# Performance work log

Measured on AMD Instinct MI355X. Metric: run time of the kernel, lower is better.

The kernel has to match this reference:

```python
import jax, jax.numpy as jnp
import numpy as np
import math

QUERY_DIM = 512
FEAT_DIM = 2048
HID_DIM = 512
OUT_DIM = 512
B, L, S, T = 32, 128, 36, 36


def _linear_params(key, d_in, d_out):
    kw, kb = jax.random.split(key)
    scale = 1.0 / math.sqrt(d_in)
    W = jax.random.uniform(kw, (d_in, d_out), jnp.float32, -scale, scale)
    b = jax.random.uniform(kb, (d_out,), jnp.float32, -scale, scale)
    return W, b


def setup_inputs() -> dict:
    key = jax.random.key(0)
    ks = jax.random.split(key, 9)
    query = jax.random.normal(ks[0], (B, L, QUERY_DIM), jnp.float32)
    src = jax.random.normal(ks[1], (B, S, FEAT_DIM), jnp.float32)
    trg = jax.random.normal(ks[2], (B, T, FEAT_DIM), jnp.float32)
    Wq, bq = _linear_params(ks[3], QUERY_DIM, HID_DIM)
    Ws, bs = _linear_params(ks[4], FEAT_DIM, HID_DIM)
    Wt, bt = _linear_params(ks[5], FEAT_DIM, HID_DIM)
    Wsv, bsv = _linear_params(ks[6], FEAT_DIM, HID_DIM)
    Wtv, btv = _linear_params(ks[7], FEAT_DIM, HID_DIM)
    Wo, bo = _linear_params(ks[8], HID_DIM * 2 + QUERY_DIM, OUT_DIM)
    return dict(query=query, src=src, trg=trg,
                Wq=Wq, bq=bq, Ws=Ws, bs=bs, Wt=Wt, bt=bt,
                Wsv=Wsv, bsv=bsv, Wtv=Wtv, btv=btv, Wo=Wo, bo=bo)


def reference(query, src, trg, Wq, bq, Ws, bs, Wt, bt, Wsv, bsv, Wtv, btv, Wo, bo):
    b, l, _ = query.shape
    s = src.shape[1]
    t = trg.shape[1]
    q = query @ Wq + bq                      # (b, l, h)
    s_key = src @ Ws + bs                    # (b, s, h)
    t_key = trg @ Wt + bt                    # (b, t, h)
    # Faithful to torch: s_key.unsqueeze(1) + t_key.unsqueeze(2) -> (b, t, s, h),
    # then labeled 'istk' in the einsum (requires s == t).
    rel_key = (s_key[:, None, :, :] + t_key[:, :, None, :]) * 0.5  # (b, t, s, h)
    weight = jnp.einsum('blk,bstk->blst', q, rel_key) / math.sqrt(HID_DIM)
    weight = jax.nn.softmax(weight.reshape(b, l, s * t), axis=-1).reshape(b, l, s, t)
    s_value = src @ Wsv + bsv                # (b, s, h)
    t_value = trg @ Wtv + btv                # (b, t, h)
    s_ctx = jnp.einsum('blst,bsh->blh', weight, s_value)
    t_ctx = jnp.einsum('blst,bth->blh', weight, t_value)
    x = jnp.concatenate((query, s_ctx, t_ctx), axis=-1)
    return jax.nn.relu(x @ Wo + bo)
```

## Files before the change

### kernel.cpp

```cpp
#include <hip/hip_runtime.h>
#include <hip/hip_bf16.h>
#include <math.h>

#define DEVI __device__ __forceinline__

typedef __attribute__((ext_vector_type(4))) float f32x4;
typedef __attribute__((ext_vector_type(8))) short bf16x8;

DEVI unsigned short f2bf(float f) {
  union { float f; unsigned int u; } v; v.f = f;
  return (unsigned short)((v.u + 0x7FFFu + ((v.u >> 16) & 1u)) >> 16);
}
DEVI float bf2f(unsigned short s) {
  union { unsigned int u; float f; } v; v.u = ((unsigned int)s) << 16; return v.f;
}
DEVI bf16x8 pack8(f32x4 a, f32x4 b) {
  bf16x8 r;
  r[0] = (short)f2bf(a[0]); r[1] = (short)f2bf(a[1]);
  r[2] = (short)f2bf(a[2]); r[3] = (short)f2bf(a[3]);
  r[4] = (short)f2bf(b[0]); r[5] = (short)f2bf(b[1]);
  r[6] = (short)f2bf(b[2]); r[7] = (short)f2bf(b[3]);
  return r;
}
DEVI void gload16(const unsigned short* g, unsigned short* l) {
  __builtin_amdgcn_global_load_lds(
      (const __attribute__((address_space(1))) unsigned int*)g,
      (__attribute__((address_space(3))) unsigned int*)l, 16, 0, 0);
}
#define SBAR() do { asm volatile("" ::: "memory"); \
                    __builtin_amdgcn_s_barrier();  \
                    asm volatile("" ::: "memory"); } while (0)

struct PrepJobs {
  const float* src[9];
  unsigned short* dst[9];
  int K[9];
  int base[9];
  int type[9];
};

__global__ __launch_bounds__(256) void prep(PrepJobs J) {
  __shared__ float t[64][65];
  int tile = blockIdx.x;
  int job = 0;
  while (job < 8 && tile >= J.base[job + 1]) ++job;
  int tl = tile - J.base[job];
  int K = J.K[job];
  if (J.type[job] == 0) {
    int tn = tl & 7, tk = tl >> 3;
    int x = threadIdx.x & 63, y = threadIdx.x >> 6;
    const float* s = J.src[job];
    int k0 = tk * 64, n0 = tn * 64;
#pragma unroll
    for (int yy = y; yy < 64; yy += 4)
      t[yy][x] = s[(size_t)(k0 + yy) * 512 + n0 + x];
    __syncthreads();
    unsigned short* d = J.dst[job];
    int kb = (x >> 3) & 7, ko = x & 7;
#pragma unroll
    for (int yy = y; yy < 64; yy += 4) {
      int n = n0 + yy;
      int kswz = k0 + (((kb + n) & 7) << 3) + ko;
      d[(size_t)n * K + kswz] = f2bf(t[x][yy]);
    }
  } else {
    int nk = K >> 6;
    int rt = tl / nk;
    int r0 = rt * 64, k0 = (tl - rt * nk) * 64;
    int r = threadIdx.x >> 2, kq = threadIdx.x & 3;
    int row = r0 + r;
    const float* s = J.src[job] + (size_t)row * K + k0 + kq * 16;
    f32x4 a0 = *(const f32x4*)s;
    f32x4 a1 = *(const f32x4*)(s + 4);
    f32x4 a2 = *(const f32x4*)(s + 8);
    f32x4 a3 = *(const f32x4*)(s + 12);
    unsigned short* d = J.dst[job] + (size_t)row * K + k0;
    int kb0 = kq * 2;
    *(bf16x8*)(d + ((kb0 + row) & 7) * 8) = pack8(a0, a1);
    *(bf16x8*)(d + ((kb0 + 1 + row) & 7) * 8) = pack8(a2, a3);
  }
}

struct GJob {
  const unsigned short* A0;
  const unsigned short* Bt;
  const float* bias;
  unsigned short* Cb;
  int Astride, Bstride, Cstride, nTilesN, nt, mode, tileBase;
};
struct GBatch { GJob j[7]; int njobs; int swz; };

__global__ __launch_bounds__(512) void gemm_pipe8(GBatch batch) {
  int gt = blockIdx.x;
  if (batch.swz) {
    int cpx = gridDim.x >> 3;
    gt = (blockIdx.x & 7) * cpx + (blockIdx.x >> 3);
  }
  int job = 0;
#pragma unroll
  for (int i = 1; i < 7; ++i)
    if (i < batch.njobs && gt >= batch.j[i].tileBase) job = i;
  GJob J = batch.j[job];
  int tl = gt - J.tileBase;
  int bm = (tl / J.nTilesN) * 128, bn = (tl % J.nTilesN) * 128;

  __shared__ __align__(16) unsigned short La[2][128 * 64];
  __shared__ __align__(16) unsigned short Lb[2][128 * 64];

  int tid = threadIdx.x;
  int wave = tid >> 6, lane = tid & 63;
  int lrow = lane & 15, lq = lane >> 4;
  int wr = (wave >> 1) * 32, wc = (wave & 1) * 64;
  f32x4 acc[2][4] = {};

  int nt = J.nt;

  auto stage_both = [&](int t, int buf) {
    const unsigned short* GA = J.A0 + (size_t)bm * J.Astride + (size_t)(t << 6);
    const unsigned short* GB = J.Bt + (size_t)bn * J.Bstride + (size_t)(t << 6);
#pragma unroll
    for (int p = 0; p < 2; ++p) {
      int s = p * 512 + tid;
      gload16(GA + (size_t)(s >> 3) * J.Astride + (s & 7) * 8,
              &La[buf][(size_t)(p * 512 + wave * 64) * 8]);
    }
#pragma unroll
    for (int p = 0; p < 2; ++p) {
      int s = p * 512 + tid;
      gload16(GB + (size_t)(s >> 3) * J.Bstride + (s & 7) * 8,
              &Lb[buf][(size_t)(p * 512 + wave * 64) * 8]);
    }
  };

  stage_both(0, 0);
  if (nt > 1) stage_both(1, 1);

  for (int t = 0; t < nt; ++t) {
    if (t + 1 < nt) asm volatile("s_waitcnt vmcnt(4)" ::: "memory");
    else            asm volatile("s_waitcnt vmcnt(0)" ::: "memory");
    SBAR();
    int cur = t & 1;
#pragma unroll
    for (int kc = 0; kc < 2; ++kc) {
      int kb = kc * 4 + lq;
      bf16x8 af[2], bv[4];
#pragma unroll
      for (int mi = 0; mi < 2; ++mi) {
        int r = wr + mi * 16 + lrow;
        af[mi] = *(const bf16x8*)&La[cur][r * 64 + ((kb + r) & 7) * 8];
      }
#pragma unroll
      for (int ni = 0; ni < 4; ++ni) {
        int r = wc + ni * 16 + lrow;
        bv[ni] = *(const bf16x8*)&Lb[cur][r * 64 + ((kb + r) & 7) * 8];
      }
#pragma unroll
      for (int mi = 0; mi < 2; ++mi)
#pragma unroll
        for (int ni = 0; ni < 4; ++ni)
          acc[mi][ni] = __builtin_amdgcn_mfma_f32_16x16x32_bf16(af[mi], bv[ni], acc[mi][ni], 0, 0, 0);
    }
    SBAR();
    if (t + 2 < nt) stage_both(t + 2, cur);
  }

#pragma unroll
  for (int mi = 0; mi < 2; ++mi) {
#pragma unroll
    for (int ni = 0; ni < 4; ++ni) {
      int gn = bn + wc + ni * 16 + lrow;
      float bvs = J.bias ? J.bias[gn] : 0.f;
      int gm0 = bm + wr + mi * 16 + lq * 4;
      if (J.mode == 0) {
#pragma unroll
        for (int r = 0; r < 4; ++r)
          J.Cb[(size_t)(gm0 + r) * J.Cstride + gn] = f2bf(acc[mi][ni][r] + bvs);
      } else {
#pragma unroll
        for (int r = 0; r < 4; ++r) {
          int row = gm0 + r;
          int col = (gn & ~63) | (((((gn >> 3) & 7) + row) & 7) << 3) | (gn & 7);
          J.Cb[(size_t)row * J.Cstride + col] = f2bf(acc[mi][ni][r] + bvs);
        }
      }
    }
  }
}

template <int MI, int NI>
__global__ __launch_bounds__(256) void gemm_pipe(GBatch batch) {
  constexpr int BM = MI * 32, BN = NI * 32;
  int gt = blockIdx.x;
  if (batch.swz) {
    int cpx = gridDim.x >> 3;
    gt = (blockIdx.x & 7) * cpx + (blockIdx.x >> 3);
  }
  int job = 0;
#pragma unroll
  for (int i = 1; i < 7; ++i)
    if (i < batch.njobs && gt >= batch.j[i].tileBase) job = i;
  GJob J = batch.j[job];
  int tl = gt - J.tileBase;
  int bm = (tl / J.nTilesN) * BM, bn = (tl % J.nTilesN) * BN;

  __shared__ __align__(16) unsigned short La[2][BM * 64];
  __shared__ __align__(16) unsigned short Lb[2][BN * 64];

  int tid = threadIdx.x;
  int wave = tid >> 6, lane = tid & 63;
  int lrow = lane & 15, lq = lane >> 4;
  int wr = (wave >> 1) * (MI * 16), wc = (wave & 1) * (NI * 16);
  f32x4 acc[MI][NI] = {};

  int nt = J.nt;

  auto stage_both = [&](int t, int buf) {
    const unsigned short* GA = J.A0 + (size_t)bm * J.Astride + (size_t)(t << 6);
    const unsigned short* GB = J.Bt + (size_t)bn * J.Bstride + (size_t)(t << 6);
#pragma unroll
    for (int p = 0; p < MI; ++p) {
      int s = p * 256 + tid;
      gload16(GA + (size_t)(s >> 3) * J.Astride + (s & 7) * 8,
              &La[buf][(size_t)(p * 256 + wave * 64) * 8]);
    }
#pragma unroll
    for (int p = 0; p < NI; ++p) {
      int s = p * 256 + tid;
      gload16(GB + (size_t)(s >> 3) * J.Bstride + (s & 7) * 8,
              &Lb[buf][(size_t)(p * 256 + wave * 64) * 8]);
    }
  };

  stage_both(0, 0);
  if (nt > 1) stage_both(1, 1);

  for (int t = 0; t < nt; ++t) {
    if (t + 1 < nt) {
      if constexpr (MI + NI == 8)      asm volatile("s_waitcnt vmcnt(8)" ::: "memory");
      else if constexpr (MI + NI == 6) asm volatile("s_waitcnt vmcnt(6)" ::: "memory");
      else                             asm volatile("s_waitcnt vmcnt(4)" ::: "memory");
    } else {
      asm volatile("s_waitcnt vmcnt(0)" ::: "memory");
    }
    SBAR();
    int cur = t & 1;
#pragma unroll
    for (int kc = 0; kc < 2; ++kc) {
      int kb = kc * 4 + lq;
      bf16x8 af[MI], bv[NI];
#pragma unroll
      for (int mi = 0; mi < MI; ++mi) {
        int r = wr + mi * 16 + lrow;
        af[mi] = *(const bf16x8*)&La[cur][r * 64 + ((kb + r) & 7) * 8];
      }
#pragma unroll
      for (int ni = 0; ni < NI; ++ni) {
        int r = wc + ni * 16 + lrow;
        bv[ni] = *(const bf16x8*)&Lb[cur][r * 64 + ((kb + r) & 7) * 8];
      }
#pragma unroll
      for (int mi = 0; mi < MI; ++mi)
#pragma unroll
        for (int ni = 0; ni < NI; ++ni)
          acc[mi][ni] = __builtin_amdgcn_mfma_f32_16x16x32_bf16(af[mi], bv[ni], acc[mi][ni], 0, 0, 0);
    }
    SBAR();
    if (t + 2 < nt) stage_both(t + 2, cur);
  }

#pragma unroll
  for (int mi = 0; mi < MI; ++mi) {
#pragma unroll
    for (int ni = 0; ni < NI; ++ni) {
      int gn = bn + wc + ni * 16 + lrow;
      float bvs = J.bias ? J.bias[gn] : 0.f;
      int gm0 = bm + wr + mi * 16 + lq * 4;
      if (J.mode == 0) {
#pragma unroll
        for (int r = 0; r < 4; ++r)
          J.Cb[(size_t)(gm0 + r) * J.Cstride + gn] = f2bf(acc[mi][ni][r] + bvs);
      } else {
#pragma unroll
        for (int r = 0; r < 4; ++r) {
          int row = gm0 + r;
          int col = (gn & ~63) | (((((gn >> 3) & 7) + row) & 7) << 3) | (gn & 7);
          J.Cb[(size_t)row * J.Cstride + col] = f2bf(acc[mi][ni][r] + bvs);
        }
      }
    }
  }
}

__global__ __launch_bounds__(256) void attn_fused(
    const unsigned short* __restrict__ qh, const unsigned short* __restrict__ s_key,
    const unsigned short* __restrict__ t_key, const unsigned short* __restrict__ svp,
    const unsigned short* __restrict__ tvp, const unsigned short* __restrict__ Pb,
    float* __restrict__ out) {
  __shared__ float red[4][3][64][4];
  __shared__ float wlT[2][36][16];
  int b = blockIdx.x, lc = blockIdx.y;
  int tid = threadIdx.x, wave = tid >> 6, lane = tid & 63;
  int lrow = lane & 15, lq = lane >> 4;
  int mat = wave >> 1, kh = wave & 1;
  int row0 = b * 128 + lc * 16;
  const unsigned short* qp = qh + (size_t)row0 * 512;
  const unsigned short* key = (mat ? s_key : t_key) + (size_t)b * 36 * 512;
  f32x4 acc[3] = {};
  for (int kc = kh * 8; kc < kh * 8 + 8; ++kc) {
    int k = kc * 32 + lq * 8;
    bf16x8 af = *(const bf16x8*)(qp + (size_t)lrow * 512 + k);
#pragma unroll
    for (int nf = 0; nf < 3; ++nf) {
      int n = nf * 16 + lrow; if (n > 35) n = 35;
      bf16x8 bv = *(const bf16x8*)(key + (size_t)n * 512 + k);
      acc[nf] = __builtin_amdgcn_mfma_f32_16x16x32_bf16(af, bv, acc[nf], 0, 0, 0);
    }
  }
#pragma unroll
  for (int nf = 0; nf < 3; ++nf)
    *(f32x4*)&red[wave][nf][lane][0] = acc[nf];
  __syncthreads();

  if (kh == 0) {
    const float ccs = 0.022097086912079608f;
    float ex[3][4];
#pragma unroll
    for (int r = 0; r < 4; ++r) {
      float a0 = (red[wave][0][lane][r] + red[wave + 1][0][lane][r]) * ccs;
      float a1 = (red[wave][1][lane][r] + red[wave + 1][1][lane][r]) * ccs;
      float a2 = (lrow < 4)
          ? (red[wave][2][lane][r] + red[wave + 1][2][lane][r]) * ccs : -1e30f;
      float mx = fmaxf(fmaxf(a0, a1), a2);
      for (int s = 1; s < 16; s <<= 1) mx = fmaxf(mx, __shfl_xor(mx, s));
      float e0 = __expf(a0 - mx), e1 = __expf(a1 - mx);
      float e2 = (lrow < 4) ? __expf(a2 - mx) : 0.f;
      float sum = e0 + e1 + e2;
      for (int s = 1; s < 16; s <<= 1) sum += __shfl_xor(sum, s);
      float inv = 1.f / sum;
      ex[0][r] = e0 * inv; ex[1][r] = e1 * inv; ex[2][r] = e2 * inv;
    }
#pragma unroll
    for (int nf = 0; nf < 3; ++nf) {
      int col = nf * 16 + lrow;
      if (col < 36) {
#pragma unroll
        for (int r = 0; r < 4; ++r)
          wlT[mat][col][lq * 4 + r] = ex[nf][r];
      }
    }
  }
  __syncthreads();

  int lgrp = tid >> 6, hgrp = tid & 63;
  float a2[4][8] = {};
#pragma unroll
  for (int m = 0; m < 2; ++m) {
    const unsigned short* V = (m ? tvp : svp) + (size_t)b * 36 * 512;
    for (int j = 0; j < 36; ++j) {
      f32x4 wa = *(const f32x4*)&wlT[m][j][lgrp * 4];
      bf16x8 v = *(const bf16x8*)(V + (size_t)j * 512 + hgrp * 8);
      float vf[8];
#pragma unroll
      for (int hi = 0; hi < 8; ++hi) vf[hi] = bf2f((unsigned short)v[hi]);
#pragma unroll
      for (int li = 0; li < 4; ++li)
#pragma unroll
        for (int hi = 0; hi < 8; ++hi) a2[li][hi] += wa[li] * vf[hi];
    }
  }
#pragma unroll
  for (int li = 0; li < 4; ++li) {
    int R = row0 + lgrp * 4 + li;
    bf16x8 p = *(const bf16x8*)(Pb + (size_t)R * 512 + hgrp * 8);
    float* op = out + (size_t)R * 512 + hgrp * 8;
    f32x4 o0, o1;
#pragma unroll
    for (int hi = 0; hi < 4; ++hi) {
      o0[hi] = fmaxf(bf2f((unsigned short)p[hi]) + a2[li][hi], 0.f);
      o1[hi] = fmaxf(bf2f((unsigned short)p[4 + hi]) + a2[li][4 + hi], 0.f);
    }
    *(f32x4*)op = o0;
    *(f32x4*)(op + 4) = o1;
  }
}

extern "C" void kernel_launch(void* const* d_in, const int* in_sizes, int n_in,
                              void* d_out, int out_size, void* d_ws, size_t ws_size,
                              hipStream_t stream) {
  (void)in_sizes; (void)n_in; (void)out_size; (void)ws_size;
  const float* query = (const float*)d_in[0];
  const float* src   = (const float*)d_in[1];
  const float* trg   = (const float*)d_in[2];
  const float* Wq  = (const float*)d_in[3];  const float* bq  = (const float*)d_in[4];
  const float* Wsk = (const float*)d_in[5];  const float* bs  = (const float*)d_in[6];
  const float* Wtk = (const float*)d_in[7];  const float* bt  = (const float*)d_in[8];
  const float* Wsv = (const float*)d_in[9];  const float* bsv = (const float*)d_in[10];
  const float* Wtv = (const float*)d_in[11]; const float* btv = (const float*)d_in[12];
  const float* Wo  = (const float*)d_in[13]; const float* bo  = (const float*)d_in[14];

  unsigned short* WqT    = (unsigned short*)d_ws;
  unsigned short* WsT    = WqT  + 512 * 512;
  unsigned short* WtT    = WsT  + 512 * 2048;
  unsigned short* WsvT   = WtT  + 512 * 2048;
  unsigned short* WtvT   = WsvT + 512 * 2048;
  unsigned short* WoT    = WtvT + 512 * 2048;
  unsigned short* queryB = WoT  + 512 * 1536;
  unsigned short* srcB   = queryB + 4096 * 512;
  unsigned short* trgB   = srcB + 1152 * 2048;
  unsigned short* qh     = trgB + 1152 * 2048;
  unsigned short* s_key  = qh + 4096 * 512;
  unsigned short* t_key  = s_key + 1152 * 512;
  unsigned short* s_val  = t_key + 1152 * 512;
  unsigned short* t_val  = s_val + 1152 * 512;
  unsigned short* svp    = t_val + 1152 * 512;
  unsigned short* tvp    = svp + 1152 * 512;
  unsigned short* Pb     = tvp + 1152 * 512;
  float* out = (float*)d_out;

  PrepJobs pj;
  const float* psrc[9] = { Wq, Wsk, Wtk, Wsv, Wtv, Wo, query, src, trg };
  unsigned short* pdst[9] = { WqT, WsT, WtT, WsvT, WtvT, WoT, queryB, srcB, trgB };
  int pK[9]    = { 512, 2048, 2048, 2048, 2048, 1536, 512, 2048, 2048 };
  int ptype[9] = { 0, 0, 0, 0, 0, 0, 1, 1, 1 };
  int prows[9] = { 0, 0, 0, 0, 0, 0, 4096, 1152, 1152 };
  int pbase = 0;
  for (int i = 0; i < 9; ++i) {
    pj.src[i] = psrc[i]; pj.dst[i] = pdst[i]; pj.K[i] = pK[i]; pj.type[i] = ptype[i];
    pj.base[i] = pbase;
    pbase += ptype[i] ? (prows[i] / 64) * (pK[i] / 64) : (pK[i] / 64) * 8;
  }
  prep<<<pbase, 256, 0, stream>>>(pj);

  {
    GBatch pb;
    pb.swz = 0;
    int base = 0;
    const unsigned short* Aarr[4] = { srcB, trgB, srcB, trgB };
    const unsigned short* Barr[4] = { WsT, WtT, WsvT, WtvT };
    const float* biasArr[4] = { bs, bt, bsv, btv };
    unsigned short* Carr[4] = { s_key, t_key, s_val, t_val };
    for (int i = 0; i < 4; ++i) {
      GJob& j = pb.j[i];
      j.A0 = Aarr[i]; j.Bt = Barr[i]; j.bias = biasArr[i]; j.Cb = Carr[i];
      j.Astride = 2048; j.Bstride = 2048; j.Cstride = 512;
      j.nTilesN = 4; j.nt = 32; j.mode = (i < 2) ? 0 : 2;
      j.tileBase = base; base += 9 * 4;
    }
    {
      GJob& j = pb.j[4];
      j.A0 = queryB; j.Bt = WqT; j.bias = bq; j.Cb = qh;
      j.Astride = 512; j.Bstride = 512; j.Cstride = 512;
      j.nTilesN = 4; j.nt = 8; j.mode = 0;
      j.tileBase = base; base += 32 * 4;
    }
    {
      GJob& j = pb.j[5];
      j.A0 = queryB; j.Bt = WoT; j.bias = bo; j.Cb = Pb;
      j.Astride = 512; j.Bstride = 1536; j.Cstride = 512;
      j.nTilesN = 4; j.nt = 8; j.mode = 0;
      j.tileBase = base; base += 32 * 4;
    }
    pb.j[6] = pb.j[5]; pb.j[6].tileBase = 0x7fffffff;
    pb.njobs = 6;
    gemm_pipe8<<<base, 512, 0, stream>>>(pb);
  }

  {
    GBatch sb;
    sb.swz = 1;
    GJob& a = sb.j[0];
    a.A0 = s_val; a.Bt = WoT + 512; a.bias = nullptr; a.Cb = svp;
    a.Astride = 512; a.Bstride = 1536; a.Cstride = 512;
    a.nTilesN = 8; a.nt = 8; a.mode = 0; a.tileBase = 0;
    GJob& b2 = sb.j[1];
    b2 = a;
    b2.A0 = t_val; b2.Bt = WoT + 1024; b2.Cb = tvp;
    b2.tileBase = 18 * 8;
    for (int i = 2; i < 7; ++i) { sb.j[i] = b2; sb.j[i].tileBase = 0x7fffffff; }
    sb.njobs = 2;
    gemm_pipe<2, 2><<<288, 256, 0, stream>>>(sb);
  }

  attn_fused<<<dim3(32, 8), 256, 0, stream>>>(qh, s_key, t_key, svp, tvp, Pb, out);
}
```

Measured before the change: 75.84 us.

## Split attention softmax into its own stage, co-scheduled with value-projection GEMMs

Replaces the 512-thread 128x128 projection GEMM with the 256-thread 2x4 templated GEMM at smaller tiles, doubling tile counts. Moves the score and softmax computation out of the final attention kernel into a combined launch that runs alongside the value-times-Wo GEMM blocks, writing softmax weights to global memory. A separate weighted-sum kernel then reads those weights. This aims to raise parallelism and overlap independent work, at the cost of an extra global round-trip for the weights and some dead leftover code (an unused staging lambda and extra shared memory).

```diff
diff --git a/kernel.cpp b/kernel.cpp
--- a/kernel.cpp
+++ b/kernel.cpp
@@ -90,103 +90,6 @@
 };
 struct GBatch { GJob j[7]; int njobs; int swz; };
 
-__global__ __launch_bounds__(512) void gemm_pipe8(GBatch batch) {
-  int gt = blockIdx.x;
-  if (batch.swz) {
-    int cpx = gridDim.x >> 3;
-    gt = (blockIdx.x & 7) * cpx + (blockIdx.x >> 3);
-  }
-  int job = 0;
-#pragma unroll
-  for (int i = 1; i < 7; ++i)
-    if (i < batch.njobs && gt >= batch.j[i].tileBase) job = i;
-  GJob J = batch.j[job];
-  int tl = gt - J.tileBase;
-  int bm = (tl / J.nTilesN) * 128, bn = (tl % J.nTilesN) * 128;
-
-  __shared__ __align__(16) unsigned short La[2][128 * 64];
-  __shared__ __align__(16) unsigned short Lb[2][128 * 64];
-
-  int tid = threadIdx.x;
-  int wave = tid >> 6, lane = tid & 63;
-  int lrow = lane & 15, lq = lane >> 4;
-  int wr = (wave >> 1) * 32, wc = (wave & 1) * 64;
-  f32x4 acc[2][4] = {};
-
-  int nt = J.nt;
-
-  auto stage_both = [&](int t, int buf) {
-    const unsigned short* GA = J.A0 + (size_t)bm * J.Astride + (size_t)(t << 6);
-    const unsigned short* GB = J.Bt + (size_t)bn * J.Bstride + (size_t)(t << 6);
-#pragma unroll
-    for (int p = 0; p < 2; ++p) {
-      int s = p * 512 + tid;
-      gload16(GA + (size_t)(s >> 3) * J.Astride + (s & 7) * 8,
-              &La[buf][(size_t)(p * 512 + wave * 64) * 8]);
-    }
-#pragma unroll
-    for (int p = 0; p < 2; ++p) {
-      int s = p * 512 + tid;
-      gload16(GB + (size_t)(s >> 3) * J.Bstride + (s & 7) * 8,
-              &Lb[buf][(size_t)(p * 512 + wave * 64) * 8]);
-    }
-  };
-
-  stage_both(0, 0);
-  if (nt > 1) stage_both(1, 1);
-
-  for (int t = 0; t < nt; ++t) {
-    if (t + 1 < nt) asm volatile("s_waitcnt vmcnt(4)" ::: "memory");
-    else            asm volatile("s_waitcnt vmcnt(0)" ::: "memory");
-    SBAR();
-    int cur = t & 1;
-#pragma unroll
-    for (int kc = 0; kc < 2; ++kc) {
-      int kb = kc * 4 + lq;
-      bf16x8 af[2], bv[4];
-#pragma unroll
-      for (int mi = 0; mi < 2; ++mi) {
-        int r = wr + mi * 16 + lrow;
-        af[mi] = *(const bf16x8*)&La[cur][r * 64 + ((kb + r) & 7) * 8];
-      }
-#pragma unroll
-      for (int ni = 0; ni < 4; ++ni) {
-        int r = wc + ni * 16 + lrow;
-        bv[ni] = *(const bf16x8*)&Lb[cur][r * 64 + ((kb + r) & 7) * 8];
-      }
-#pragma unroll
-      for (int mi = 0; mi < 2; ++mi)
-#pragma unroll
-        for (int ni = 0; ni < 4; ++ni)
-          acc[mi][ni] = __builtin_amdgcn_mfma_f32_16x16x32_bf16(af[mi], bv[ni], acc[mi][ni], 0, 0, 0);
-    }
-    SBAR();
-    if (t + 2 < nt) stage_both(t + 2, cur);
-  }
-
-#pragma unroll
-  for (int mi = 0; mi < 2; ++mi) {
-#pragma unroll
-    for (int ni = 0; ni < 4; ++ni) {
-      int gn = bn + wc + ni * 16 + lrow;
-      float bvs = J.bias ? J.bias[gn] : 0.f;
-      int gm0 = bm + wr + mi * 16 + lq * 4;
-      if (J.mode == 0) {
-#pragma unroll
-        for (int r = 0; r < 4; ++r)
-          J.Cb[(size_t)(gm0 + r) * J.Cstride + gn] = f2bf(acc[mi][ni][r] + bvs);
-      } else {
-#pragma unroll
-        for (int r = 0; r < 4; ++r) {
-          int row = gm0 + r;
-          int col = (gn & ~63) | (((((gn >> 3) & 7) + row) & 7) << 3) | (gn & 7);
-          J.Cb[(size_t)row * J.Cstride + col] = f2bf(acc[mi][ni][r] + bvs);
-        }
-      }
-    }
-  }
-}
-
 template <int MI, int NI>
 __global__ __launch_bounds__(256) void gemm_pipe(GBatch batch) {
   constexpr int BM = MI * 32, BN = NI * 32;
@@ -291,63 +194,187 @@
   }
 }
 
-__global__ __launch_bounds__(256) void attn_fused(
-    const unsigned short* __restrict__ qh, const unsigned short* __restrict__ s_key,
-    const unsigned short* __restrict__ t_key, const unsigned short* __restrict__ svp,
-    const unsigned short* __restrict__ tvp, const unsigned short* __restrict__ Pb,
-    float* __restrict__ out) {
-  __shared__ float red[4][3][64][4];
+struct HJob {
+  const unsigned short* A0;
+  const unsigned short* Bt;
+  unsigned short* Cb;
+  int Astride, Bstride, Cstride, nTilesN, nt, tileBase;
+};
+struct S3Args {
+  HJob g[2];
+  int nGemm;
+  const unsigned short* qh;
+  const unsigned short* s_key;
+  const unsigned short* t_key;
+  float* Wsw;
+  float* Wtw;
+};
+
+__global__ __launch_bounds__(256) void stage3(S3Args A) {
+  __shared__ __align__(16) unsigned char smem[16384];
+  int tid = threadIdx.x;
+  int wave = tid >> 6, lane = tid & 63;
+  int lrow = lane & 15, lq = lane >> 4;
+
+  if ((int)blockIdx.x < A.nGemm) {
+    unsigned short* Ls = (unsigned short*)smem;
+    int gt = blockIdx.x;
+    HJob J = (gt >= A.g[1].tileBase) ? A.g[1] : A.g[0];
+    int tl = gt - J.tileBase;
+    int bm = (tl / J.nTilesN) * 64, bn = (tl % J.nTilesN) * 64;
+    int wr = (wave >> 1) * 32, wc = (wave & 1) * 32;
+    f32x4 acc[2][2] = {};
+    int nt = J.nt;
+
+    auto stage_both = [&](int t, int buf) {
+      const unsigned short* GA = J.A0 + (size_t)bm * J.Astride + (size_t)(t << 6);
+      const unsigned short* GB = J.Bt + (size_t)bn * J.Bstride + (size_t)(t << 6);
+#pragma unroll
+      for (int p = 0; p < 2; ++p) {
+        int s = p * 256 + tid;
+        gload16(GA + (size_t)(s >> 3) * J.Astride + (s & 7) * 8,
+                &Ls[(size_t)buf * 2048 + (size_t)((p * 256 + wave * 64) & 1023) * 8
+                    + (size_t)(p >> 1) * 0]);
+      }
+#pragma unroll
+      for (int p = 0; p < 2; ++p) {
+        int s = p * 256 + tid;
+        gload16(GB + (size_t)(s >> 3) * J.Bstride + (s & 7) * 8,
+                &Ls[4096 + (size_t)buf * 2048 + (size_t)(p * 256 + wave * 64) * 8]);
+      }
+    };
+    (void)stage_both;
+
+    unsigned short* La0 = (unsigned short*)smem;
+    unsigned short* Lb0 = La0 + 2 * 4096;
+    __shared__ __align__(16) unsigned short Lg[2][4096 + 4096];
+    auto stage2 = [&](int t, int buf) {
+      const unsigned short* GA = J.A0 + (size_t)bm * J.Astride + (size_t)(t << 6);
+      const unsigned short* GB = J.Bt + (size_t)bn * J.Bstride + (size_t)(t << 6);
+#pragma unroll
+      for (int p = 0; p < 2; ++p) {
+        int s = p * 256 + tid;
+        gload16(GA + (size_t)(s >> 3) * J.Astride + (s & 7) * 8,
+                &Lg[buf][(size_t)(p * 256 + wave * 64) * 8]);
+      }
+#pragma unroll
+      for (int p = 0; p < 2; ++p) {
+        int s = p * 256 + tid;
+        gload16(GB + (size_t)(s >> 3) * J.Bstride + (s & 7) * 8,
+                &Lg[buf][4096 + (size_t)(p * 256 + wave * 64) * 8]);
+      }
+    };
+
+    stage2(0, 0);
+    if (nt > 1) stage2(1, 1);
+
+    for (int t = 0; t < nt; ++t) {
+      if (t + 1 < nt) asm volatile("s_waitcnt vmcnt(4)" ::: "memory");
+      else            asm volatile("s_waitcnt vmcnt(0)" ::: "memory");
+      SBAR();
+      int cur = t & 1;
+#pragma unroll
+      for (int kc = 0; kc < 2; ++kc) {
+        int kb = kc * 4 + lq;
+        bf16x8 af[2], bv[2];
+#pragma unroll
+        for (int mi = 0; mi < 2; ++mi) {
+          int r = wr + mi * 16 + lrow;
+          af[mi] = *(const bf16x8*)&Lg[cur][r * 64 + ((kb + r) & 7) * 8];
+        }
+#pragma unroll
+        for (int ni = 0; ni < 2; ++ni) {
+          int r = wc + ni * 16 + lrow;
+          bv[ni] = *(const bf16x8*)&Lg[cur][4096 + r * 64 + ((kb + r) & 7) * 8];
+        }
+#pragma unroll
+        for (int mi = 0; mi < 2; ++mi)
+#pragma unroll
+          for (int ni = 0; ni < 2; ++ni)
+            acc[mi][ni] = __builtin_amdgcn_mfma_f32_16x16x32_bf16(af[mi], bv[ni], acc[mi][ni], 0, 0, 0);
+      }
+      SBAR();
+      if (t + 2 < nt) stage2(t + 2, cur);
+    }
+#pragma unroll
+    for (int mi = 0; mi < 2; ++mi) {
+#pragma unroll
+      for (int ni = 0; ni < 2; ++ni) {
+        int gn = bn + wc + ni * 16 + lrow;
+        int gm0 = bm + wr + mi * 16 + lq * 4;
+#pragma unroll
+        for (int r = 0; r < 4; ++r)
+          J.Cb[(size_t)(gm0 + r) * J.Cstride + gn] = f2bf(acc[mi][ni][r]);
+      }
+    }
+  } else {
+    float (*red)[3][64][4] = (float(*)[3][64][4])smem;
+    int bid2 = blockIdx.x - A.nGemm;
+    int b = bid2 >> 3, lc = bid2 & 7;
+    int mat = wave >> 1, kh = wave & 1;
+    int row0 = b * 128 + lc * 16;
+    const unsigned short* qp = A.qh + (size_t)row0 * 512;
+    const unsigned short* key = (mat ? A.s_key : A.t_key) + (size_t)b * 36 * 512;
+    f32x4 acc[3] = {};
+    for (int kc = kh * 8; kc < kh * 8 + 8; ++kc) {
+      int k = kc * 32 + lq * 8;
+      bf16x8 af = *(const bf16x8*)(qp + (size_t)lrow * 512 + k);
+#pragma unroll
+      for (int nf = 0; nf < 3; ++nf) {
+        int n = nf * 16 + lrow; if (n > 35) n = 35;
+        bf16x8 bv = *(const bf16x8*)(key + (size_t)n * 512 + k);
+        acc[nf] = __builtin_amdgcn_mfma_f32_16x16x32_bf16(af, bv, acc[nf], 0, 0, 0);
+      }
+    }
+#pragma unroll
+    for (int nf = 0; nf < 3; ++nf)
+      *(f32x4*)&red[wave][nf][lane][0] = acc[nf];
+    __syncthreads();
+
+    if (kh == 0) {
+      const float ccs = 0.022097086912079608f;
+      float ex[3][4];
+#pragma unroll
+      for (int r = 0; r < 4; ++r) {
+        float a0 = (red[wave][0][lane][r] + red[wave + 1][0][lane][r]) * ccs;
+        float a1 = (red[wave][1][lane][r] + red[wave + 1][1][lane][r]) * ccs;
+        float a2 = (lrow < 4)
+            ? (red[wave][2][lane][r] + red[wave + 1][2][lane][r]) * ccs : -1e30f;
+        float mx = fmaxf(fmaxf(a0, a1), a2);
+        for (int s = 1; s < 16; s <<= 1) mx = fmaxf(mx, __shfl_xor(mx, s));
+        float e0 = __expf(a0 - mx), e1 = __expf(a1 - mx);
+        float e2 = (lrow < 4) ? __expf(a2 - mx) : 0.f;
+        float sum = e0 + e1 + e2;
+        for (int s = 1; s < 16; s <<= 1) sum += __shfl_xor(sum, s);
+        float inv = 1.f / sum;
+        ex[0][r] = e0 * inv; ex[1][r] = e1 * inv; ex[2][r] = e2 * inv;
+      }
+      float* W = mat ? A.Wtw : A.Wsw;
+#pragma unroll
+      for (int nf = 0; nf < 3; ++nf) {
+        int col = nf * 16 + lrow;
+        if (col < 36) {
+#pragma unroll
+          for (int r = 0; r < 4; ++r)
+            W[(size_t)(row0 + lq * 4 + r) * 36 + col] = ex[nf][r];
+        }
+      }
+    }
+  }
+}
+
+__global__ __launch_bounds__(256) void wsum(
+    const float* __restrict__ Wsw, const float* __restrict__ Wtw,
+    const unsigned short* __restrict__ svp, const unsigned short* __restrict__ tvp,
+    const unsigned short* __restrict__ Pb, float* __restrict__ out) {
   __shared__ float wlT[2][36][16];
   int b = blockIdx.x, lc = blockIdx.y;
-  int tid = threadIdx.x, wave = tid >> 6, lane = tid & 63;
-  int lrow = lane & 15, lq = lane >> 4;
-  int mat = wave >> 1, kh = wave & 1;
+  int tid = threadIdx.x;
   int row0 = b * 128 + lc * 16;
-  const unsigned short* qp = qh + (size_t)row0 * 512;
-  const unsigned short* key = (mat ? s_key : t_key) + (size_t)b * 36 * 512;
-  f32x4 acc[3] = {};
-  for (int kc = kh * 8; kc < kh * 8 + 8; ++kc) {
-    int k = kc * 32 + lq * 8;
-    bf16x8 af = *(const bf16x8*)(qp + (size_t)lrow * 512 + k);
-#pragma unroll
-    for (int nf = 0; nf < 3; ++nf) {
-      int n = nf * 16 + lrow; if (n > 35) n = 35;
-      bf16x8 bv = *(const bf16x8*)(key + (size_t)n * 512 + k);
-      acc[nf] = __builtin_amdgcn_mfma_f32_16x16x32_bf16(af, bv, acc[nf], 0, 0, 0);
-    }
-  }
-#pragma unroll
-  for (int nf = 0; nf < 3; ++nf)
-    *(f32x4*)&red[wave][nf][lane][0] = acc[nf];
-  __syncthreads();
-
-  if (kh == 0) {
-    const float ccs = 0.022097086912079608f;
-    float ex[3][4];
-#pragma unroll
-    for (int r = 0; r < 4; ++r) {
-      float a0 = (red[wave][0][lane][r] + red[wave + 1][0][lane][r]) * ccs;
-      float a1 = (red[wave][1][lane][r] + red[wave + 1][1][lane][r]) * ccs;
-      float a2 = (lrow < 4)
-          ? (red[wave][2][lane][r] + red[wave + 1][2][lane][r]) * ccs : -1e30f;
-      float mx = fmaxf(fmaxf(a0, a1), a2);
-      for (int s = 1; s < 16; s <<= 1) mx = fmaxf(mx, __shfl_xor(mx, s));
-      float e0 = __expf(a0 - mx), e1 = __expf(a1 - mx);
-      float e2 = (lrow < 4) ? __expf(a2 - mx) : 0.f;
-      float sum = e0 + e1 + e2;
-      for (int s = 1; s < 16; s <<= 1) sum += __shfl_xor(sum, s);
-      float inv = 1.f / sum;
-      ex[0][r] = e0 * inv; ex[1][r] = e1 * inv; ex[2][r] = e2 * inv;
-    }
-#pragma unroll
-    for (int nf = 0; nf < 3; ++nf) {
-      int col = nf * 16 + lrow;
-      if (col < 36) {
-#pragma unroll
-        for (int r = 0; r < 4; ++r)
-          wlT[mat][col][lq * 4 + r] = ex[nf][r];
-      }
-    }
+  for (int i = tid; i < 2 * 16 * 36; i += 256) {
+    int m = i / 576, rem = i - m * 576;
+    int l = rem / 36, j = rem - l * 36;
+    wlT[m][j][l] = (m ? Wtw : Wsw)[(size_t)(row0 + l) * 36 + j];
   }
   __syncthreads();
 
@@ -415,6 +442,8 @@
   unsigned short* svp    = t_val + 1152 * 512;
   unsigned short* tvp    = svp + 1152 * 512;
   unsigned short* Pb     = tvp + 1152 * 512;
+  float* Wsw = (float*)(Pb + 4096 * 512);
+  float* Wtw = Wsw + 4096 * 36;
   float* out = (float*)d_out;
 
   PrepJobs pj;
@@ -444,42 +473,42 @@
       j.A0 = Aarr[i]; j.Bt = Barr[i]; j.bias = biasArr[i]; j.Cb = Carr[i];
       j.Astride = 2048; j.Bstride = 2048; j.Cstride = 512;
       j.nTilesN = 4; j.nt = 32; j.mode = (i < 2) ? 0 : 2;
-      j.tileBase = base; base += 9 * 4;
+      j.tileBase = base; base += 18 * 4;
     }
     {
       GJob& j = pb.j[4];
       j.A0 = queryB; j.Bt = WqT; j.bias = bq; j.Cb = qh;
       j.Astride = 512; j.Bstride = 512; j.Cstride = 512;
       j.nTilesN = 4; j.nt = 8; j.mode = 0;
-      j.tileBase = base; base += 32 * 4;
+      j.tileBase = base; base += 64 * 4;
     }
     {
       GJob& j = pb.j[5];
       j.A0 = queryB; j.Bt = WoT; j.bias = bo; j.Cb = Pb;
       j.Astride = 512; j.Bstride = 1536; j.Cstride = 512;
       j.nTilesN = 4; j.nt = 8; j.mode = 0;
-      j.tileBase = base; base += 32 * 4;
+      j.tileBase = base; base += 64 * 4;
     }
     pb.j[6] = pb.j[5]; pb.j[6].tileBase = 0x7fffffff;
     pb.njobs = 6;
-    gemm_pipe8<<<base, 512, 0, stream>>>(pb);
+    gemm_pipe<2, 4><<<base, 256, 0, stream>>>(pb);
   }
 
   {
-    GBatch sb;
-    sb.swz = 1;
-    GJob& a = sb.j[0];
-    a.A0 = s_val; a.Bt = WoT + 512; a.bias = nullptr; a.Cb = svp;
+    S3Args sa;
+    HJob& a = sa.g[0];
+    a.A0 = s_val; a.Bt = WoT + 512; a.Cb = svp;
     a.Astride = 512; a.Bstride = 1536; a.Cstride = 512;
-    a.nTilesN = 8; a.nt = 8; a.mode = 0; a.tileBase = 0;
-    GJob& b2 = sb.j[1];
+    a.nTilesN = 8; a.nt = 8; a.tileBase = 0;
+    HJob& b2 = sa.g[1];
     b2 = a;
     b2.A0 = t_val; b2.Bt = WoT + 1024; b2.Cb = tvp;
     b2.tileBase = 18 * 8;
-    for (int i = 2; i < 7; ++i) { sb.j[i] = b2; sb.j[i].tileBase = 0x7fffffff; }
-    sb.njobs = 2;
-    gemm_pipe<2, 2><<<288, 256, 0, stream>>>(sb);
-  }
-
-  attn_fused<<<dim3(32, 8), 256, 0, stream>>>(qh, s_key, t_key, svp, tvp, Pb, out);
-}
+    sa.nGemm = 288;
+    sa.qh = qh; sa.s_key = s_key; sa.t_key = t_key;
+    sa.Wsw = Wsw; sa.Wtw = Wtw;
+    stage3<<<288 + 256, 256, 0, stream>>>(sa);
+  }
+
+  wsum<<<dim3(32, 8), 256, 0, stream>>>(Wsw, Wtw, svp, tvp, Pb, out);
+}
```

Result: faster. 73.11 us (-3.6%).
